# Kernel tuning notes

Measured on AMD Instinct MI355X. Metric: run time of the kernel, lower is better.

Reference implementation:

```python
import jax, jax.numpy as jnp
import numpy as np
from jax import lax

BN_EPS = 1e-3  # keras BatchNormalization default epsilon
TOP_K = 2      # keep_top_k


def _conv3(x, k, b, s):
    # x: NDHWC, k: DHWIO, 'SAME' padding like keras Conv3D(padding='same')
    y = lax.conv_general_dilated(x, k, (s, s, s), 'SAME',
                                 dimension_numbers=('NDHWC', 'DHWIO', 'NDHWC'))
    return y + b


def _bn(x, g, be, m, v):
    # inference-mode batch norm with moving statistics
    return g * (x - m) * lax.rsqrt(v + BN_EPS) + be


def setup_inputs() -> dict:
    key = jax.random.key(0)
    ks = jax.random.split(key, 64)
    B, S = 16, 96
    nf, ksz, nE, nb = 32, 3, 8, 4
    inp = {"x": jax.random.normal(ks[0], (B, S, S, S, 1), jnp.float32)}
    cin = 1
    for i in range(nb):
        cout = nf * 2 ** i
        base = 1 + 6 * i
        inp["k%d" % i] = jax.random.normal(ks[base], (ksz, ksz, ksz, cin, cout), jnp.float32) * 0.05
        inp["b%d" % i] = jnp.zeros((cout,), jnp.float32)
        inp["g%d" % i] = 1.0 + 0.1 * jax.random.normal(ks[base + 1], (cout,), jnp.float32)
        inp["be%d" % i] = 0.1 * jax.random.normal(ks[base + 2], (cout,), jnp.float32)
        inp["m%d" % i] = 0.1 * jax.random.normal(ks[base + 3], (cout,), jnp.float32)
        inp["v%d" % i] = jax.random.uniform(ks[base + 4], (cout,), jnp.float32, 0.5, 1.5)
        cin = cout
    c = nf * 2 ** (nb - 1)  # 256
    inp["w1k"] = jax.random.normal(ks[30], (1, 1, 1, c, c), jnp.float32) * 0.05
    inp["w1b"] = jnp.zeros((c,), jnp.float32)
    inp["wg"] = 1.0 + 0.1 * jax.random.normal(ks[31], (c,), jnp.float32)
    inp["wbe"] = 0.1 * jax.random.normal(ks[32], (c,), jnp.float32)
    inp["wm"] = 0.1 * jax.random.normal(ks[33], (c,), jnp.float32)
    inp["wv"] = jax.random.uniform(ks[34], (c,), jnp.float32, 0.5, 1.5)
    inp["w2k"] = jax.random.normal(ks[35], (1, 1, 1, c, nE), jnp.float32) * 0.05
    inp["w2b"] = jnp.zeros((nE,), jnp.float32)
    return inp


def reference(x, k0, b0, g0, be0, m0, v0, k1, b1, g1, be1, m1, v1,
              k2, b2, g2, be2, m2, v2, k3, b3, g3, be3, m3, v3,
              w1k, w1b, wg, wbe, wm, wv, w2k, w2b):
    blocks = [(k0, b0, g0, be0, m0, v0), (k1, b1, g1, be1, m1, v1),
              (k2, b2, g2, be2, m2, v2), (k3, b3, g3, be3, m3, v3)]
    h = x
    for k, b, g, be, m, v in blocks:  # EncoderBlock: Conv3D(stride 2)+BN+ReLU
        h = jax.nn.relu(_bn(_conv3(h, k, b, 2), g, be, m, v))
    h = jnp.mean(h, axis=(1, 2, 3), keepdims=True)  # GAP, [B,1,1,1,256]
    w = _conv3(h, w1k, w1b, 1)
    w = jax.nn.relu(_bn(w, wg, wbe, wm, wv))
    w = _conv3(w, w2k, w2b, 1)  # [B,1,1,1,n_experts]
    # noisy-top-k gating (noise disabled at inference): mask non-top-k to -inf
    top_vals = lax.top_k(w, TOP_K)[0]
    thr = top_vals[..., TOP_K - 1:TOP_K]
    w = jnp.where(w >= thr, w, -jnp.inf)
    return jax.nn.softmax(w, axis=-1)
```

## Files before the change

### kernel.cpp

```cpp
#include <hip/hip_runtime.h>
#include <math.h>

#define BN_EPS 1e-3f

typedef __attribute__((ext_vector_type(8))) unsigned short ushort8v;
typedef __attribute__((ext_vector_type(8))) short short8v;
typedef __attribute__((ext_vector_type(4))) float f32x4;
typedef __attribute__((ext_vector_type(4))) unsigned int uint4v;

__device__ __forceinline__ float4 f4load(const float* p) {
    return *reinterpret_cast<const float4*>(p);
}
__device__ __forceinline__ float bf2f(unsigned short u) {
    union { unsigned int i; float f; } w; w.i = ((unsigned int)u) << 16; return w.f;
}
__device__ __forceinline__ unsigned short f2bf(float f) {
    union { float fv; unsigned int i; } w; w.fv = f;
    unsigned int lsb = (w.i >> 16) & 1u;
    w.i += 0x7fffu + lsb;
    return (unsigned short)(w.i >> 16);
}
__device__ __forceinline__ unsigned cvtpk(float lo, float hi) {
    unsigned r;
    asm("v_cvt_pk_bf16_f32 %0, %1, %2" : "=v"(r) : "v"(lo), "v"(hi));
    return r;
}
__device__ __forceinline__ void st_pair(unsigned short* p0, unsigned short* p1,
                                        float f0, float f1) {
    unsigned u = cvtpk(f0, f1);
    p0[0] = (unsigned short)u;
    p1[0] = (unsigned short)(u >> 16);
}
template<int N> __device__ __forceinline__ void waitv() {
    asm volatile("s_waitcnt vmcnt(%0)" :: "n"(N) : "memory");
}

#define GLOAD_LDS16(g, l)                                                     \
    __builtin_amdgcn_global_load_lds(                                         \
        (const __attribute__((address_space(1))) void*)(const void*)(g),      \
        (__attribute__((address_space(3))) void*)(void*)(l), 16, 0, 0)

template<int CIN, int COUT>
__device__ __forceinline__ void wprep_body(
    const float* __restrict__ k, unsigned short* __restrict__ wt, int blk)
{
    constexpr int NS = COUT / 16;
    constexpr int KS = CIN / 32;
    int idx = blk * 256 + (int)threadIdx.x;
    if (idx >= 27 * KS * NS * 64) return;
    int lane = idx & 63;
    int nsg  = (idx >> 6) % NS;
    int it   = idx / (64 * NS);
    int tap  = it / KS;
    int ks   = it - tap * KS;
    int sg = lane >> 4, lr = lane & 15;
    int cout = nsg * 16 + lr;
    ushort8v o;
    #pragma unroll
    for (int j = 0; j < 8; ++j) {
        int ci = ks * 32 + sg * 8 + j;
        o[j] = f2bf(k[(size_t)(tap * CIN + ci) * COUT + cout]);
    }
    *reinterpret_cast<ushort8v*>(wt + (size_t)idx * 8) = o;
}

__global__ __launch_bounds__(256) void wprep_all(
    const float* __restrict__ k0,
    const float* __restrict__ k1, const float* __restrict__ k2, const float* __restrict__ k3,
    unsigned short* __restrict__ w0f,
    unsigned short* __restrict__ w1, unsigned short* __restrict__ w2, unsigned short* __restrict__ w3,
    unsigned short* __restrict__ zp)
{
    int b = blockIdx.x;
    if (b < 27)       wprep_body<32, 64>(k1, w1, b);
    else if (b < 135) wprep_body<64, 128>(k2, w2, b - 27);
    else if (b < 567) wprep_body<128, 256>(k3, w3, b - 135);
    else {
        reinterpret_cast<unsigned int*>(zp)[threadIdx.x] = 0u;
        if (threadIdx.x < 128) {
            int ns = threadIdx.x >> 6, lane = threadIdx.x & 63;
            int sg = lane >> 4, lr = lane & 15;
            ushort8v o;
            #pragma unroll
            for (int j = 0; j < 8; ++j) {
                int t = sg * 8 + j;
                o[j] = (t < 27) ? f2bf(k0[t * 32 + ns * 16 + lr]) : (unsigned short)0;
            }
            *reinterpret_cast<ushort8v*>(w0f + (ns * 64 + lane) * 8) = o;
        }
    }
}

__global__ __launch_bounds__(256) void conv0_mfma(
    const float* __restrict__ x, const unsigned short* __restrict__ w0f,
    const float* __restrict__ zf,
    const float* __restrict__ b, const float* __restrict__ g,
    const float* __restrict__ be, const float* __restrict__ m,
    const float* __restrict__ v, unsigned short* __restrict__ y)
{
    const int l   = threadIdx.x & 63;
    const int wid = threadIdx.x >> 6;
    const int sg  = l >> 4;
    const int lr  = l & 15;
    const int vwave = (blockIdx.x * 4 + wid) * 64;

    const short8v B0 = *(const short8v*)(w0f + l * 8);
    const short8v B1 = *(const short8v*)(w0f + (64 + l) * 8);

    int offs[8];
    #pragma unroll
    for (int j = 0; j < 8; ++j) {
        int t = sg * 8 + j;
        int kd = t / 9, r9 = t - kd * 9, kh = r9 / 3, kw = r9 - kh * 3;
        offs[j] = (kd * 96 + kh) * 96 + kw;
    }

    const float* ap0[4];
    unsigned m8[4];
    #pragma unroll
    for (int mi = 0; mi < 4; ++mi) {
        int vA = vwave + mi * 16 + lr;
        int ow = vA % 48; int t1 = vA / 48;
        int oh = t1 % 48; int t2 = t1 / 48;
        int od = t2 % 48; int n  = t2 / 48;
        ap0[mi] = x + ((size_t)(n * 96 + 2 * od) * 96 + 2 * oh) * 96 + 2 * ow;
        unsigned sm = ((od == 47) ? 0x07FC0000u : 0u)
                    | ((oh == 47) ? 0x070381C0u : 0u)
                    | ((ow == 47) ? 0x04924924u : 0u);
        m8[mi] = ((sm >> (sg * 8)) & 0xFFu) | ((sg == 3) ? 0xF8u : 0u);
    }

    float av[4][8];
    #pragma unroll
    for (int mi = 0; mi < 4; ++mi)
        #pragma unroll
        for (int j = 0; j < 8; ++j) {
            const float* p = ((m8[mi] >> j) & 1u) ? zf : (ap0[mi] + offs[j]);
            av[mi][j] = *p;
        }

    f32x4 acc[4][2];
    #pragma unroll
    for (int mi = 0; mi < 4; ++mi) {
        acc[mi][0] = (f32x4){0.f, 0.f, 0.f, 0.f};
        acc[mi][1] = (f32x4){0.f, 0.f, 0.f, 0.f};
    }
    #pragma unroll
    for (int mi = 0; mi < 4; ++mi) {
        uint4v au;
        au[0] = cvtpk(av[mi][0], av[mi][1]);
        au[1] = cvtpk(av[mi][2], av[mi][3]);
        au[2] = cvtpk(av[mi][4], av[mi][5]);
        au[3] = cvtpk(av[mi][6], av[mi][7]);
        short8v a = __builtin_bit_cast(short8v, au);
        acc[mi][0] = __builtin_amdgcn_mfma_f32_16x16x32_bf16(a, B0, acc[mi][0], 0, 0, 0);
        acc[mi][1] = __builtin_amdgcn_mfma_f32_16x16x32_bf16(a, B1, acc[mi][1], 0, 0, 0);
    }

    float S[2], T[2];
    #pragma unroll
    for (int ns = 0; ns < 2; ++ns) {
        int c = ns * 16 + lr;
        float sc = g[c] * rsqrtf(v[c] + BN_EPS);
        S[ns] = sc;
        T[ns] = (b[c] - m[c]) * sc + be[c];
    }
    #pragma unroll
    for (int mi = 0; mi < 4; ++mi) {
        #pragma unroll
        for (int i = 0; i < 4; i += 2) {
            int vD0 = vwave + mi * 16 + sg * 4 + i;
            unsigned short* yp0 = y + (size_t)vD0 * 32;
            unsigned short* yp1 = yp0 + 32;
            st_pair(yp0 + lr, yp1 + lr,
                    fmaxf(acc[mi][0][i]     * S[0] + T[0], 0.f),
                    fmaxf(acc[mi][0][i + 1] * S[0] + T[0], 0.f));
            st_pair(yp0 + 16 + lr, yp1 + 16 + lr,
                    fmaxf(acc[mi][1][i]     * S[1] + T[1], 0.f),
                    fmaxf(acc[mi][1][i + 1] * S[1] + T[1], 0.f));
        }
    }
}

template<int CIN, int COUT, int INS, int OUTS, int MW, int NSW, int NH,
         int CSPLIT, int KU>
__global__ __launch_bounds__(256, 2) void conv_mfma_lds(
    const unsigned short* __restrict__ x, const unsigned short* __restrict__ wt,
    const unsigned short* __restrict__ zp,
    const float* __restrict__ b, const float* __restrict__ g,
    const float* __restrict__ be, const float* __restrict__ m,
    const float* __restrict__ v, unsigned short* __restrict__ y)
{
    constexpr int NSfull = COUT / 16;
    constexpr int NSB = NSW * NH;
    constexpr int KS = CIN / 32;
    constexpr int NITK = 27 * KS;
    constexpr int NIT = NITK / KU;
    constexpr int MGROUPS = 4 / NH;
    constexpr int MTILE = MGROUPS * MW * 16;
    constexpr int BSTEP = NSB * KU * 1024;
    constexpr int ASTEP = MGROUPS * MW * KU * 1024;
    constexpr int STRIDE = BSTEP + ASTEP;
    constexpr int BL = (NSB * KU) / 4;
    constexpr int AL = MW * KU;
    static_assert(NSB * CSPLIT == NSfull && NITK % KU == 0 && (NSB * KU) % 4 == 0, "tiling");
    static_assert(NIT >= 3, "pipeline depth");

    __shared__ __attribute__((aligned(16))) char lds[3 * STRIDE];

    const int l   = threadIdx.x & 63;
    const int wid = threadIdx.x >> 6;
    const int sg  = l >> 4;
    const int lr  = l & 15;

    const int mblk   = blockIdx.x / CSPLIT;
    const int cchunk = blockIdx.x % CSPLIT;
    const int mgroup = wid / NH;
    const int ngroup = wid % NH;
    const int gCoutBase = (cchunk * NSB + ngroup * NSW) * 16;
    const int vwave = mblk * MTILE + mgroup * MW * 16;

    const unsigned short* ap0[MW];
    unsigned smask[MW];
    #pragma unroll
    for (int mi = 0; mi < MW; ++mi) {
        int vA = vwave + mi * 16 + lr;
        int owA = vA % OUTS; int t1 = vA / OUTS;
        int ohA = t1 % OUTS; int t2 = t1 / OUTS;
        int odA = t2 % OUTS; int nA = t2 / OUTS;
        ap0[mi] = x + ((((size_t)nA * INS + 2 * odA) * INS + 2 * ohA) * INS + 2 * owA) * CIN + sg * 8;
        smask[mi] = ((odA == OUTS - 1) ? 0x07FC0000u : 0u)
                  | ((ohA == OUTS - 1) ? 0x070381C0u : 0u)
                  | ((owA == OUTS - 1) ? 0x04924924u : 0u);
    }

    const unsigned short* zpl = (const unsigned short*)((const char*)zp + l * 16);

    f32x4 acc[MW][NSW];
    #pragma unroll
    for (int mi = 0; mi < MW; ++mi)
        #pragma unroll
        for (int ns = 0; ns < NSW; ++ns) acc[mi][ns] = (f32x4){0.f, 0.f, 0.f, 0.f};

    auto stage = [&](int ito, int p) {
        char* dst = &lds[p * STRIDE];
        #pragma unroll
        for (int c = 0; c < BL; ++c) {
            int idx  = c * 256 + (int)threadIdx.x;
            int lane = idx & 63;
            int sub  = idx >> 6;
            int u    = sub / NSB;
            int grp  = sub % NSB;
            int it   = ito * KU + u;
            const unsigned short* src =
                wt + ((size_t)(it * NSfull + cchunk * NSB + grp) * 64 + lane) * 8;
            GLOAD_LDS16(src, dst + sub * 1024);
        }
        if (ngroup == 0) {
            #pragma unroll
            for (int u = 0; u < KU; ++u) {
                int it = ito * KU + u;
                int tap = (KS == 1) ? it : it / KS;
                int ks  = (KS == 1) ? 0  : it - tap * KS;
                int kd = tap / 9, r9 = tap - kd * 9, kh = r9 / 3, kw = r9 - kh * 3;
                size_t aoff = (size_t)((kd * INS + kh) * INS + kw) * CIN + ks * 32;
                #pragma unroll
                for (int mi = 0; mi < MW; ++mi) {
                    const unsigned short* ga =
                        ((smask[mi] >> tap) & 1u) ? zpl : (ap0[mi] + aoff);
                    GLOAD_LDS16(ga, dst + BSTEP + ((mgroup * MW + mi) * KU + u) * 1024);
                }
            }
        }
    };

    auto computestep = [&](const char* buf) {
        #pragma unroll
        for (int u = 0; u < KU; ++u) {
            short8v Bf[NSW], Af[MW];
            #pragma unroll
            for (int ns = 0; ns < NSW; ++ns)
                Bf[ns] = *(const short8v*)(buf + (u * NSB + ngroup * NSW + ns) * 1024 + l * 16);
            #pragma unroll
            for (int mi = 0; mi < MW; ++mi)
                Af[mi] = *(const short8v*)(buf + BSTEP + ((mgroup * MW + mi) * KU + u) * 1024 + l * 16);
            #pragma unroll
            for (int mi = 0; mi < MW; ++mi)
                #pragma unroll
                for (int ns = 0; ns < NSW; ++ns)
                    acc[mi][ns] = __builtin_amdgcn_mfma_f32_16x16x32_bf16(Af[mi], Bf[ns], acc[mi][ns], 0, 0, 0);
        }
    };

    stage(0, 0);
    stage(1, 1);
    #pragma unroll 1
    for (int ito = 0; ito < NIT - 1; ++ito) {
        if (ngroup == 0) waitv<BL + AL>(); else waitv<BL>();
        __builtin_amdgcn_s_barrier();
        asm volatile("" ::: "memory");
        if (ito + 2 < NIT) stage(ito + 2, (ito + 2) % 3);
        computestep(&lds[(ito % 3) * STRIDE]);
    }
    waitv<0>();
    __builtin_amdgcn_s_barrier();
    asm volatile("" ::: "memory");
    computestep(&lds[((NIT - 1) % 3) * STRIDE]);

    float S[NSW], T[NSW];
    #pragma unroll
    for (int ns = 0; ns < NSW; ++ns) {
        int c = gCoutBase + ns * 16 + lr;
        float sc = g[c] * rsqrtf(v[c] + BN_EPS);
        S[ns] = sc;
        T[ns] = (b[c] - m[c]) * sc + be[c];
    }
    #pragma unroll
    for (int mi = 0; mi < MW; ++mi) {
        #pragma unroll
        for (int i = 0; i < 4; i += 2) {
            int vD0 = vwave + mi * 16 + sg * 4 + i;
            int vD1 = vD0 + 1;
            int ow0 = vD0 % OUTS; int u1 = vD0 / OUTS;
            int oh0 = u1 % OUTS; int u2 = u1 / OUTS;
            int od0 = u2 % OUTS; int n0 = u2 / OUTS;
            unsigned short* yp0 =
                y + ((((size_t)n0 * OUTS + od0) * OUTS + oh0) * OUTS + ow0) * COUT + gCoutBase + lr;
            int ow1 = vD1 % OUTS; int w1 = vD1 / OUTS;
            int oh1 = w1 % OUTS; int w2 = w1 / OUTS;
            int od1 = w2 % OUTS; int n1 = w2 / OUTS;
            unsigned short* yp1 =
                y + ((((size_t)n1 * OUTS + od1) * OUTS + oh1) * OUTS + ow1) * COUT + gCoutBase + lr;
            #pragma unroll
            for (int ns = 0; ns < NSW; ++ns)
                st_pair(yp0 + ns * 16, yp1 + ns * 16,
                        fmaxf(acc[mi][ns][i]     * S[ns] + T[ns], 0.f),
                        fmaxf(acc[mi][ns][i + 1] * S[ns] + T[ns], 0.f));
        }
    }
}

__global__ __launch_bounds__(256) void head_kernel(
    const unsigned short* __restrict__ x4,
    const float* __restrict__ w1k, const float* __restrict__ w1b,
    const float* __restrict__ wg,  const float* __restrict__ wbe,
    const float* __restrict__ wm,  const float* __restrict__ wv,
    const float* __restrict__ w2k, const float* __restrict__ w2b,
    float* __restrict__ out)
{
    __shared__ float part[8][256];
    __shared__ float h[256];
    __shared__ float r[256];
    __shared__ float logits[8];

    const int n = blockIdx.x;
    const int t = threadIdx.x;
    const int c8 = t & 31;
    const int pg = t >> 5;

    const unsigned short* xb = x4 + (size_t)n * 216 * 256 + c8 * 8;
    float s[8] = {0.f, 0.f, 0.f, 0.f, 0.f, 0.f, 0.f, 0.f};
    for (int i = pg; i < 216; i += 8) {
        ushort8v v8 = *reinterpret_cast<const ushort8v*>(xb + (size_t)i * 256);
        #pragma unroll
        for (int j = 0; j < 8; ++j) s[j] += bf2f(v8[j]);
    }
    #pragma unroll
    for (int j = 0; j < 8; ++j) part[pg][c8 * 8 + j] = s[j];
    __syncthreads();

    float a = 0.f;
    #pragma unroll
    for (int gi = 0; gi < 8; ++gi) a += part[gi][t];
    h[t] = a * (1.0f / 216.0f);
    __syncthreads();

    float acc = w1b[t];
    #pragma unroll 4
    for (int ci = 0; ci < 256; ++ci) acc += h[ci] * w1k[ci * 256 + t];
    float sc = wg[t] * rsqrtf(wv[t] + BN_EPS);
    acc = (acc - wm[t]) * sc + wbe[t];
    r[t] = fmaxf(acc, 0.f);
    __syncthreads();

    if (t < 8) {
        float a2 = w2b[t];
        for (int ci = 0; ci < 256; ++ci) a2 += r[ci] * w2k[ci * 8 + t];
        logits[t] = a2;
    }
    __syncthreads();

    if (t == 0) {
        float m1 = -INFINITY, m2 = -INFINITY;
        for (int e = 0; e < 8; ++e) {
            float val = logits[e];
            if (val > m1) { m2 = m1; m1 = val; }
            else if (val > m2) { m2 = val; }
        }
        float thr = m2;
        float ex[8]; float sum = 0.f;
        for (int e = 0; e < 8; ++e) {
            float val = (logits[e] >= thr) ? logits[e] : -INFINITY;
            ex[e] = expf(val - m1);
            sum += ex[e];
        }
        float inv = 1.0f / sum;
        for (int e = 0; e < 8; ++e) out[n * 8 + e] = ex[e] * inv;
    }
}

extern "C" void kernel_launch(void* const* d_in, const int* in_sizes, int n_in,
                              void* d_out, int out_size, void* d_ws, size_t ws_size,
                              hipStream_t stream) {
    const float* x   = (const float*)d_in[0];
    const float* k0  = (const float*)d_in[1];
    const float* b0  = (const float*)d_in[2];
    const float* g0  = (const float*)d_in[3];
    const float* be0 = (const float*)d_in[4];
    const float* m0  = (const float*)d_in[5];
    const float* v0  = (const float*)d_in[6];
    const float* k1  = (const float*)d_in[7];
    const float* b1  = (const float*)d_in[8];
    const float* g1  = (const float*)d_in[9];
    const float* be1 = (const float*)d_in[10];
    const float* m1  = (const float*)d_in[11];
    const float* v1  = (const float*)d_in[12];
    const float* k2  = (const float*)d_in[13];
    const float* b2  = (const float*)d_in[14];
    const float* g2  = (const float*)d_in[15];
    const float* be2 = (const float*)d_in[16];
    const float* m2  = (const float*)d_in[17];
    const float* v2  = (const float*)d_in[18];
    const float* k3  = (const float*)d_in[19];
    const float* b3  = (const float*)d_in[20];
    const float* g3  = (const float*)d_in[21];
    const float* be3 = (const float*)d_in[22];
    const float* m3  = (const float*)d_in[23];
    const float* v3  = (const float*)d_in[24];
    const float* w1k = (const float*)d_in[25];
    const float* w1b = (const float*)d_in[26];
    const float* wg  = (const float*)d_in[27];
    const float* wbe = (const float*)d_in[28];
    const float* wm  = (const float*)d_in[29];
    const float* wv  = (const float*)d_in[30];
    const float* w2k = (const float*)d_in[31];
    const float* w2b = (const float*)d_in[32];

    unsigned short* x1  = (unsigned short*)d_ws;
    unsigned short* x2  = x1 + 56623104;
    unsigned short* x3  = x2 + 14155776;
    unsigned short* x4  = x3 + 3538944;
    unsigned short* Wt1 = x4 + 884736;
    unsigned short* Wt2 = Wt1 + 55296;
    unsigned short* Wt3 = Wt2 + 221184;
    unsigned short* zp  = Wt3 + 884736;
    unsigned short* W0f = zp + 512;

    wprep_all<<<568, 256, 0, stream>>>(k0, k1, k2, k3, W0f, Wt1, Wt2, Wt3, zp);
    conv0_mfma<<<6912, 256, 0, stream>>>(x, W0f, (const float*)zp, b0, g0, be0, m0, v0, x1);
    conv_mfma_lds<32, 64, 48, 24, 2, 4, 1, 1, 1><<<1728, 256, 0, stream>>>(x1, Wt1, zp, b1, g1, be1, m1, v1, x2);
    conv_mfma_lds<64, 128, 24, 12, 1, 4, 2, 1, 1><<<864, 256, 0, stream>>>(x2, Wt2, zp, b2, g2, be2, m2, v2, x3);
    conv_mfma_lds<128, 256, 12, 6, 1, 1, 4, 4, 2><<<864, 256, 0, stream>>>(x3, Wt3, zp, b3, g3, be3, m3, v3, x4);
    head_kernel<<<16, 256, 0, stream>>>(x4, w1k, w1b, wg, wbe, wm, wv, w2k, w2b, (float*)d_out);
}
```

Measured before the change: 199.8 us.

## Stage conv0 input tile in LDS via async global-to-LDS loads

Rewrites the first stride-2 conv to load a 9x9x33 input patch per block into shared memory using coalesced 16-byte global_load_lds transfers, plus a side column. Taps are then gathered from LDS instead of issuing scattered scalar global loads per tap. The block-to-output mapping is changed to 4x4x16 spatial tiles so neighbouring outputs share the staged data. This adds a barrier and LDS bank conflicts from the stride-2 reads.

```diff
diff --git a/kernel.cpp b/kernel.cpp
--- a/kernel.cpp
+++ b/kernel.cpp
@@ -39,6 +39,10 @@
     __builtin_amdgcn_global_load_lds(                                         \
         (const __attribute__((address_space(1))) void*)(const void*)(g),      \
         (__attribute__((address_space(3))) void*)(void*)(l), 16, 0, 0)
+#define GLOAD_LDS4(g, l)                                                      \
+    __builtin_amdgcn_global_load_lds(                                         \
+        (const __attribute__((address_space(1))) void*)(const void*)(g),      \
+        (__attribute__((address_space(3))) void*)(void*)(l), 4, 0, 0)
 
 template<int CIN, int COUT>
 __device__ __forceinline__ void wprep_body(
@@ -91,53 +95,73 @@
     }
 }
 
-__global__ __launch_bounds__(256) void conv0_mfma(
+__global__ __launch_bounds__(256) void conv0_lds(
     const float* __restrict__ x, const unsigned short* __restrict__ w0f,
     const float* __restrict__ zf,
     const float* __restrict__ b, const float* __restrict__ g,
     const float* __restrict__ be, const float* __restrict__ m,
     const float* __restrict__ v, unsigned short* __restrict__ y)
 {
+    __shared__ __attribute__((aligned(16))) float tile[81 * 32];
+    __shared__ float side[84];
+    __shared__ float zslot;
+
     const int l   = threadIdx.x & 63;
     const int wid = threadIdx.x >> 6;
     const int sg  = l >> 4;
     const int lr  = l & 15;
-    const int vwave = (blockIdx.x * 4 + wid) * 64;
+
+    int bb = blockIdx.x;
+    const int owt = bb % 3;  bb /= 3;
+    const int oht = bb % 12; bb /= 12;
+    const int odt = bb % 12; const int n = bb / 12;
+
+    const int id0 = odt * 8, ih0 = oht * 8, iw0 = owt * 32;
+
+    if (threadIdx.x == 0) zslot = 0.f;
+
+    #pragma unroll
+    for (int q0 = 0; q0 < 648; q0 += 256) {
+        int qq = q0 + wid * 64;
+        int q = qq + l;
+        if (qq < 648 && q < 648) {
+            int row = q >> 3, c = q & 7;
+            int dd = row / 9, hh = row - dd * 9;
+            int id = id0 + dd, ih = ih0 + hh;
+            const float* src = (id < 96 && ih < 96)
+                ? x + ((size_t)(n * 96 + id) * 96 + ih) * 96 + iw0 + c * 4
+                : zf;
+            GLOAD_LDS16(src, (char*)tile + (size_t)qq * 16);
+        }
+    }
+    {
+        int row = (wid == 0) ? l : ((wid == 1 && l < 17) ? 64 + l : -1);
+        if (row >= 0) {
+            int dd = row / 9, hh = row - dd * 9;
+            int id = id0 + dd, ih = ih0 + hh;
+            const float* src = (id < 96 && ih < 96 && iw0 + 32 < 96)
+                ? x + ((size_t)(n * 96 + id) * 96 + ih) * 96 + iw0 + 32
+                : zf;
+            GLOAD_LDS4(src, (char*)side + (wid == 0 ? 0 : 256));
+        }
+    }
+    __syncthreads();
 
     const short8v B0 = *(const short8v*)(w0f + l * 8);
     const short8v B1 = *(const short8v*)(w0f + (64 + l) * 8);
 
-    int offs[8];
+    int ej[8], wwj[8];
+    bool validj[8], sidej[8];
     #pragma unroll
     for (int j = 0; j < 8; ++j) {
-        int t = sg * 8 + j;
+        int tap = sg * 8 + j;
+        int t = (tap < 27) ? tap : 0;
         int kd = t / 9, r9 = t - kd * 9, kh = r9 / 3, kw = r9 - kh * 3;
-        offs[j] = (kd * 96 + kh) * 96 + kw;
-    }
-
-    const float* ap0[4];
-    unsigned m8[4];
-    #pragma unroll
-    for (int mi = 0; mi < 4; ++mi) {
-        int vA = vwave + mi * 16 + lr;
-        int ow = vA % 48; int t1 = vA / 48;
-        int oh = t1 % 48; int t2 = t1 / 48;
-        int od = t2 % 48; int n  = t2 / 48;
-        ap0[mi] = x + ((size_t)(n * 96 + 2 * od) * 96 + 2 * oh) * 96 + 2 * ow;
-        unsigned sm = ((od == 47) ? 0x07FC0000u : 0u)
-                    | ((oh == 47) ? 0x070381C0u : 0u)
-                    | ((ow == 47) ? 0x04924924u : 0u);
-        m8[mi] = ((sm >> (sg * 8)) & 0xFFu) | ((sg == 3) ? 0xF8u : 0u);
-    }
-
-    float av[4][8];
-    #pragma unroll
-    for (int mi = 0; mi < 4; ++mi)
-        #pragma unroll
-        for (int j = 0; j < 8; ++j) {
-            const float* p = ((m8[mi] >> j) & 1u) ? zf : (ap0[mi] + offs[j]);
-            av[mi][j] = *p;
-        }
+        ej[j] = kd * 9 + kh;
+        wwj[j] = 2 * lr + kw;
+        sidej[j] = (wwj[j] >= 32);
+        validj[j] = (tap < 27);
+    }
 
     f32x4 acc[4][2];
     #pragma unroll
@@ -145,13 +169,22 @@
         acc[mi][0] = (f32x4){0.f, 0.f, 0.f, 0.f};
         acc[mi][1] = (f32x4){0.f, 0.f, 0.f, 0.f};
     }
+
     #pragma unroll
     for (int mi = 0; mi < 4; ++mi) {
+        float av[8];
+        #pragma unroll
+        for (int j = 0; j < 8; ++j) {
+            int row = 18 * wid + 2 * mi + ej[j];
+            const float* p = sidej[j] ? &side[row] : &tile[row * 32 + wwj[j]];
+            p = validj[j] ? p : &zslot;
+            av[j] = *p;
+        }
         uint4v au;
-        au[0] = cvtpk(av[mi][0], av[mi][1]);
-        au[1] = cvtpk(av[mi][2], av[mi][3]);
-        au[2] = cvtpk(av[mi][4], av[mi][5]);
-        au[3] = cvtpk(av[mi][6], av[mi][7]);
+        au[0] = cvtpk(av[0], av[1]);
+        au[1] = cvtpk(av[2], av[3]);
+        au[2] = cvtpk(av[4], av[5]);
+        au[3] = cvtpk(av[6], av[7]);
         short8v a = __builtin_bit_cast(short8v, au);
         acc[mi][0] = __builtin_amdgcn_mfma_f32_16x16x32_bf16(a, B0, acc[mi][0], 0, 0, 0);
         acc[mi][1] = __builtin_amdgcn_mfma_f32_16x16x32_bf16(a, B1, acc[mi][1], 0, 0, 0);
@@ -165,12 +198,15 @@
         S[ns] = sc;
         T[ns] = (b[c] - m[c]) * sc + be[c];
     }
+    const int odG = odt * 4 + wid;
     #pragma unroll
     for (int mi = 0; mi < 4; ++mi) {
+        int oh = oht * 4 + mi;
+        unsigned short* yrow =
+            y + (((size_t)(n * 48 + odG) * 48 + oh) * 48 + owt * 16) * 32;
         #pragma unroll
         for (int i = 0; i < 4; i += 2) {
-            int vD0 = vwave + mi * 16 + sg * 4 + i;
-            unsigned short* yp0 = y + (size_t)vD0 * 32;
+            unsigned short* yp0 = yrow + (size_t)(sg * 4 + i) * 32;
             unsigned short* yp1 = yp0 + 32;
             st_pair(yp0 + lr, yp1 + lr,
                     fmaxf(acc[mi][0][i]     * S[0] + T[0], 0.f),
@@ -457,7 +493,7 @@
     unsigned short* W0f = zp + 512;
 
     wprep_all<<<568, 256, 0, stream>>>(k0, k1, k2, k3, W0f, Wt1, Wt2, Wt3, zp);
-    conv0_mfma<<<6912, 256, 0, stream>>>(x, W0f, (const float*)zp, b0, g0, be0, m0, v0, x1);
+    conv0_lds<<<6912, 256, 0, stream>>>(x, W0f, (const float*)zp, b0, g0, be0, m0, v0, x1);
     conv_mfma_lds<32, 64, 48, 24, 2, 4, 1, 1, 1><<<1728, 256, 0, stream>>>(x1, Wt1, zp, b1, g1, be1, m1, v1, x2);
     conv_mfma_lds<64, 128, 24, 12, 1, 4, 2, 1, 1><<<864, 256, 0, stream>>>(x2, Wt2, zp, b2, g2, be2, m2, v2, x3);
     conv_mfma_lds<128, 256, 12, 6, 1, 1, 4, 4, 2><<<864, 256, 0, stream>>>(x3, Wt3, zp, b3, g3, be3, m3, v3, x4);
```

After: 195.8 us. 2.0% less time.
